# Performance work log

Measured on AMD Instinct MI355X. Metric: run time of the kernel, lower is better.

Reference implementation:

```python
import jax, jax.numpy as jnp
import numpy as np


def setup_inputs() -> dict:
    key = jax.random.key(0)
    kA, kB = jax.random.split(key)
    B, H, W, C = 8, 48, 48, 256
    feature_A = jax.random.normal(kA, (B, H, W, C), dtype=jnp.float32)
    feature_B = jax.random.normal(kB, (B, H, W, C), dtype=jnp.float32)
    return {"feature_A": feature_A, "feature_B": feature_B}


def reference(feature_A, feature_B):
    # corr[b,i,j,k,l] = mean_c A[b,i,j,c] * B[b,k,l,c]
    # Expressed as a batched GEMM over the channel dim instead of the
    # naive [B,H,W,H,W,C] broadcast intermediate.
    C = feature_A.shape[-1]
    corr = jnp.einsum('bijc,bklc->bijkl', feature_A, feature_B) / C
    # L2 norm over source positions (i,j) per target position (k,l)
    penalty = jnp.sqrt(jnp.sum(corr * corr, axis=(1, 2), keepdims=True))  # [B,1,1,H,W]
    return corr / penalty
```

## Files before the change

### kernel.cpp

```cpp
#include <hip/hip_runtime.h>
#include <hip/hip_bf16.h>


#define HW2 2304
#define CH  256
#define NB  8
#define NELEM (NB * HW2 * CH)

typedef __attribute__((ext_vector_type(8))) short bf16x8;
typedef __attribute__((ext_vector_type(4))) float f32x4;

static __device__ inline unsigned short f2bf(float f) {
    union { float f; unsigned u; } x; x.f = f;
    unsigned r = x.u + 0x7FFFu + ((x.u >> 16) & 1u);
    return (unsigned short)(r >> 16);
}

static __device__ inline void async_copy16(const void* g, void* l) {
    __builtin_amdgcn_global_load_lds(
        (const __attribute__((address_space(1))) unsigned int*)g,
        (__attribute__((address_space(3))) unsigned int*)l, 16, 0, 0);
}

__global__ __launch_bounds__(256) void convert_bf16(const float* __restrict__ A,
                                                    const float* __restrict__ B,
                                                    unsigned short* __restrict__ Abf,
                                                    unsigned short* __restrict__ Bbf) {
    const int n4 = NELEM / 4;
    for (int i = blockIdx.x * blockDim.x + threadIdx.x; i < 2 * n4;
         i += gridDim.x * blockDim.x) {
        const bool isA = i < n4;
        const int j = isA ? i : i - n4;
        float4 v = (isA ? (const float4*)A : (const float4*)B)[j];
        ushort4 p;
        p.x = f2bf(v.x); p.y = f2bf(v.y); p.z = f2bf(v.z); p.w = f2bf(v.w);
        *(ushort4*)((isA ? Abf : Bbf) + (size_t)j * 4) = p;
    }
}

template <bool WRITE_OUT>
__global__ __launch_bounds__(256) void corr_pass(const unsigned short* __restrict__ Abf,
                                                 const unsigned short* __restrict__ Bbf,
                                                 float* __restrict__ colSqG,
                                                 float* __restrict__ out) {
    __shared__ unsigned short As[2 * 128 * 32];
    __shared__ unsigned short Bs[2 * 128 * 32];
    __shared__ float colSq[128];

    const int tid = threadIdx.x;

    const int lin = blockIdx.x + 18 * (blockIdx.y + 18 * blockIdx.z);
    const int b  = lin & 7;
    const int r_ = lin >> 3;
    const int bx = r_ % 18;
    const int by = r_ / 18;

    if (!WRITE_OUT && tid < 128) colSq[tid] = 0.0f;

    const unsigned short* Ab = Abf + ((size_t)b * HW2 + (size_t)by * 128) * CH;
    const unsigned short* Bb = Bbf + ((size_t)b * HW2 + (size_t)bx * 128) * CH;

    const int srow  = tid >> 2;
    const int skcol = (tid & 3) * 8;

    const int wave = tid >> 6;
    const int lane = tid & 63;
    const int wm   = (wave >> 1) * 64;
    const int wn   = (wave & 1) * 64;
    const int lr   = lane & 15;
    const int quad = lane >> 4;
    const int k8   = quad * 8;

    f32x4 acc[4][4];
#pragma unroll
    for (int i = 0; i < 4; i++)
#pragma unroll
        for (int j = 0; j < 4; j++) acc[i][j] = (f32x4){0.f, 0.f, 0.f, 0.f};

    for (int kt = 0; kt < CH; kt += 64) {
#pragma unroll
        for (int c = 0; c < 2; c++) {
            const int kof = kt + c * 32;
#pragma unroll
            for (int i = 0; i < 2; i++) {
                async_copy16(Ab + (size_t)(srow + i * 64) * CH + kof + skcol,
                             &As[c * 4096 + tid * 8 + i * 2048]);
                async_copy16(Bb + (size_t)(srow + i * 64) * CH + kof + skcol,
                             &Bs[c * 4096 + tid * 8 + i * 2048]);
            }
        }
        __syncthreads();

#pragma unroll
        for (int c = 0; c < 2; c++) {
            bf16x8 af[4], bfr[4];
#pragma unroll
            for (int mt = 0; mt < 4; mt++)
                af[mt] = *(const bf16x8*)&As[c * 4096 + (wm + mt * 16 + lr) * 32 + k8];
#pragma unroll
            for (int nt = 0; nt < 4; nt++)
                bfr[nt] = *(const bf16x8*)&Bs[c * 4096 + (wn + nt * 16 + lr) * 32 + k8];
#pragma unroll
            for (int mt = 0; mt < 4; mt++)
#pragma unroll
                for (int nt = 0; nt < 4; nt++)
                    acc[mt][nt] = __builtin_amdgcn_mfma_f32_16x16x32_bf16(
                        af[mt], bfr[nt], acc[mt][nt], 0, 0, 0);
        }
        __syncthreads();
    }

    const int colBase = bx * 128 + wn;
    if (!WRITE_OUT) {
#pragma unroll
        for (int nt = 0; nt < 4; nt++) {
            float s = 0.f;
#pragma unroll
            for (int mt = 0; mt < 4; mt++) {
                f32x4 v = acc[mt][nt];
#pragma unroll
                for (int r = 0; r < 4; r++) s += v[r] * v[r];
            }
            s += __shfl_xor(s, 16);
            s += __shfl_xor(s, 32);
            if (quad == 0) atomicAdd(&colSq[wn + nt * 16 + lr], s);
        }
        __syncthreads();
        if (tid < 128)
            atomicAdd(&colSqG[(size_t)b * HW2 + bx * 128 + tid], colSq[tid]);
    } else {
        const size_t outBase = (size_t)b * HW2 * HW2;
#pragma unroll
        for (int nt = 0; nt < 4; nt++) {
            const int col = colBase + nt * 16 + lr;
            const float rinv = rsqrtf(colSqG[(size_t)b * HW2 + col]);
#pragma unroll
            for (int mt = 0; mt < 4; mt++) {
                const int row0 = by * 128 + wm + mt * 16 + quad * 4;
                f32x4 v = acc[mt][nt];
#pragma unroll
                for (int r = 0; r < 4; r++)
                    out[outBase + (size_t)(row0 + r) * HW2 + col] = v[r] * rinv;
            }
        }
    }
}

extern "C" void kernel_launch(void* const* d_in, const int* in_sizes, int n_in,
                              void* d_out, int out_size, void* d_ws, size_t ws_size,
                              hipStream_t stream) {
    const float* A = (const float*)d_in[0];
    const float* B = (const float*)d_in[1];
    float* out = (float*)d_out;

    unsigned short* Abf = (unsigned short*)d_ws;
    unsigned short* Bbf = Abf + NELEM;
    float* colSqG = (float*)(Bbf + NELEM);

    hipMemsetAsync(colSqG, 0, (size_t)NB * HW2 * sizeof(float), stream);
    convert_bf16<<<2048, 256, 0, stream>>>(A, B, Abf, Bbf);

    dim3 grid(HW2 / 128, HW2 / 128, NB);
    corr_pass<false><<<grid, 256, 0, stream>>>(Abf, Bbf, colSqG, out);
    corr_pass<true><<<grid, 256, 0, stream>>>(Abf, Bbf, colSqG, out);
}
```

Measured before the change: 237.5 us.

## Compute column norms via Gram matrix A^T A instead of full correlation pass

Replaces the first full HW×HW correlation GEMM used for column sum of squares with an algebraic identity: ||A b_k||^2 = b_k^T (A^T A) b_k. The convert kernel now also writes a transposed bf16 copy of A, a split-K kernel builds the 256×256 Gram matrix per batch with atomics, and a small GEMM of B against the Gram matrix gives the column norms. This removes roughly half of the MFMA work, at the cost of extra kernels, a transposed copy, and rounding the Gram matrix to bf16, which may reduce the accuracy of the norms.

After: 254.5 us. 7.2% more time.

```diff
diff --git a/kernel.cpp b/kernel.cpp
--- a/kernel.cpp
+++ b/kernel.cpp
@@ -1,11 +1,11 @@
 #include <hip/hip_runtime.h>
-#include <hip/hip_bf16.h>
 
 
 #define HW2 2304
 #define CH  256
 #define NB  8
 #define NELEM (NB * HW2 * CH)
+#define KS  6
 
 typedef __attribute__((ext_vector_type(8))) short bf16x8;
 typedef __attribute__((ext_vector_type(4))) float f32x4;
@@ -16,6 +16,11 @@
     return (unsigned short)(r >> 16);
 }
 
+static __device__ inline float bf2f(unsigned short u) {
+    union { unsigned u; float f; } x; x.u = ((unsigned)u) << 16;
+    return x.f;
+}
+
 static __device__ inline void async_copy16(const void* g, void* l) {
     __builtin_amdgcn_global_load_lds(
         (const __attribute__((address_space(1))) unsigned int*)g,
@@ -25,28 +30,203 @@
 __global__ __launch_bounds__(256) void convert_bf16(const float* __restrict__ A,
                                                     const float* __restrict__ B,
                                                     unsigned short* __restrict__ Abf,
-                                                    unsigned short* __restrict__ Bbf) {
-    const int n4 = NELEM / 4;
-    for (int i = blockIdx.x * blockDim.x + threadIdx.x; i < 2 * n4;
-         i += gridDim.x * blockDim.x) {
-        const bool isA = i < n4;
-        const int j = isA ? i : i - n4;
-        float4 v = (isA ? (const float4*)A : (const float4*)B)[j];
-        ushort4 p;
-        p.x = f2bf(v.x); p.y = f2bf(v.y); p.z = f2bf(v.z); p.w = f2bf(v.w);
-        *(ushort4*)((isA ? Abf : Bbf) + (size_t)j * 4) = p;
-    }
-}
-
-template <bool WRITE_OUT>
-__global__ __launch_bounds__(256) void corr_pass(const unsigned short* __restrict__ Abf,
-                                                 const unsigned short* __restrict__ Bbf,
-                                                 float* __restrict__ colSqG,
-                                                 float* __restrict__ out) {
+                                                    unsigned short* __restrict__ Bbf,
+                                                    unsigned short* __restrict__ Atbf) {
+    __shared__ unsigned short t[64][65];
+    const int blk = blockIdx.x;
+    const bool isA = blk < 1152;
+    const int tb = isA ? blk : blk - 1152;
+    const int b  = tb / 144;
+    const int tt = tb % 144;
+    const int ijt = tt >> 2, ct = tt & 3;
+    const size_t base = ((size_t)b * HW2 + (size_t)ijt * 64) * CH + ct * 64;
+    const float* src = (isA ? A : B) + base;
+    unsigned short* dst = (isA ? Abf : Bbf) + base;
+    const int tid = threadIdx.x;
+    const int lr = tid & 15, rq = tid >> 4;
+#pragma unroll
+    for (int p = 0; p < 4; p++) {
+        const int row = rq + p * 16;
+        float4 v = *(const float4*)(src + (size_t)row * CH + lr * 4);
+        ushort4 u;
+        u.x = f2bf(v.x); u.y = f2bf(v.y); u.z = f2bf(v.z); u.w = f2bf(v.w);
+        *(ushort4*)(dst + (size_t)row * CH + lr * 4) = u;
+        if (isA) {
+            t[row][lr * 4 + 0] = u.x; t[row][lr * 4 + 1] = u.y;
+            t[row][lr * 4 + 2] = u.z; t[row][lr * 4 + 3] = u.w;
+        }
+    }
+    if (isA) {
+        __syncthreads();
+#pragma unroll
+        for (int p = 0; p < 4; p++) {
+            const int c = rq + p * 16;
+            ushort4 u;
+            u.x = t[lr * 4 + 0][c]; u.y = t[lr * 4 + 1][c];
+            u.z = t[lr * 4 + 2][c]; u.w = t[lr * 4 + 3][c];
+            *(ushort4*)(Atbf + ((size_t)b * CH + (size_t)(ct * 64 + c)) * HW2
+                        + (size_t)ijt * 64 + lr * 4) = u;
+        }
+    }
+}
+
+__global__ __launch_bounds__(256) void gram_partial(const unsigned short* __restrict__ Atbf,
+                                                    float* __restrict__ Gf) {
     __shared__ unsigned short As[2 * 128 * 32];
     __shared__ unsigned short Bs[2 * 128 * 32];
-    __shared__ float colSq[128];
-
+    const int tid = threadIdx.x;
+    const int bx = blockIdx.x, by = blockIdx.y;
+    const int b  = blockIdx.z / KS, ks = blockIdx.z % KS;
+    const int kt0 = ks * (HW2 / KS);
+
+    const unsigned short* Ar = Atbf + ((size_t)b * CH + by * 128) * HW2;
+    const unsigned short* Br = Atbf + ((size_t)b * CH + bx * 128) * HW2;
+
+    const int srow = tid >> 2, skcol = (tid & 3) * 8;
+    const int wave = tid >> 6, lane = tid & 63;
+    const int wm = (wave >> 1) * 64, wn = (wave & 1) * 64;
+    const int lr = lane & 15, quad = lane >> 4, k8 = quad * 8;
+
+    f32x4 acc[4][4];
+#pragma unroll
+    for (int i = 0; i < 4; i++)
+#pragma unroll
+        for (int j = 0; j < 4; j++) acc[i][j] = (f32x4){0.f, 0.f, 0.f, 0.f};
+
+    for (int kt = kt0; kt < kt0 + HW2 / KS; kt += 64) {
+#pragma unroll
+        for (int c = 0; c < 2; c++) {
+            const int kof = kt + c * 32;
+#pragma unroll
+            for (int i = 0; i < 2; i++) {
+                async_copy16(Ar + (size_t)(srow + i * 64) * HW2 + kof + skcol,
+                             &As[c * 4096 + tid * 8 + i * 2048]);
+                async_copy16(Br + (size_t)(srow + i * 64) * HW2 + kof + skcol,
+                             &Bs[c * 4096 + tid * 8 + i * 2048]);
+            }
+        }
+        __syncthreads();
+#pragma unroll
+        for (int c = 0; c < 2; c++) {
+            bf16x8 af[4], bfr[4];
+#pragma unroll
+            for (int mt = 0; mt < 4; mt++)
+                af[mt] = *(const bf16x8*)&As[c * 4096 + (wm + mt * 16 + lr) * 32 + k8];
+#pragma unroll
+            for (int nt = 0; nt < 4; nt++)
+                bfr[nt] = *(const bf16x8*)&Bs[c * 4096 + (wn + nt * 16 + lr) * 32 + k8];
+#pragma unroll
+            for (int mt = 0; mt < 4; mt++)
+#pragma unroll
+                for (int nt = 0; nt < 4; nt++)
+                    acc[mt][nt] = __builtin_amdgcn_mfma_f32_16x16x32_bf16(
+                        af[mt], bfr[nt], acc[mt][nt], 0, 0, 0);
+        }
+        __syncthreads();
+    }
+#pragma unroll
+    for (int mt = 0; mt < 4; mt++)
+#pragma unroll
+        for (int nt = 0; nt < 4; nt++) {
+            f32x4 v = acc[mt][nt];
+            const int row = by * 128 + wm + mt * 16 + quad * 4;
+            const int col = bx * 128 + wn + nt * 16 + lr;
+#pragma unroll
+            for (int r = 0; r < 4; r++)
+                atomicAdd(&Gf[((size_t)b * CH + row + r) * CH + col], v[r]);
+        }
+}
+
+__global__ __launch_bounds__(256) void g_to_bf(const float* __restrict__ Gf,
+                                               unsigned short* __restrict__ Gbf) {
+    const int i = blockIdx.x * 256 + threadIdx.x;
+    float4 v = ((const float4*)Gf)[i];
+    ushort4 u;
+    u.x = f2bf(v.x); u.y = f2bf(v.y); u.z = f2bf(v.z); u.w = f2bf(v.w);
+    ((ushort4*)Gbf)[i] = u;
+}
+
+__global__ __launch_bounds__(256) void colsq_pass(const unsigned short* __restrict__ Bbf,
+                                                  const unsigned short* __restrict__ Gbf,
+                                                  float* __restrict__ colSqG) {
+    __shared__ unsigned short As[2 * 128 * 32];
+    __shared__ unsigned short Bs[2 * 128 * 32];
+    const int tid = threadIdx.x;
+    const int bx = blockIdx.x;
+    const int by = blockIdx.y;
+    const int b  = blockIdx.z;
+
+    const unsigned short* Ab = Bbf + ((size_t)b * HW2 + by * 128) * CH;
+    const unsigned short* Gb = Gbf + ((size_t)b * CH + bx * 128) * CH;
+
+    const int srow = tid >> 2, skcol = (tid & 3) * 8;
+    const int wave = tid >> 6, lane = tid & 63;
+    const int wm = (wave >> 1) * 64, wn = (wave & 1) * 64;
+    const int lr = lane & 15, quad = lane >> 4, k8 = quad * 8;
+
+    f32x4 acc[4][4];
+#pragma unroll
+    for (int i = 0; i < 4; i++)
+#pragma unroll
+        for (int j = 0; j < 4; j++) acc[i][j] = (f32x4){0.f, 0.f, 0.f, 0.f};
+
+    for (int kt = 0; kt < CH; kt += 64) {
+#pragma unroll
+        for (int c = 0; c < 2; c++) {
+            const int kof = kt + c * 32;
+#pragma unroll
+            for (int i = 0; i < 2; i++) {
+                async_copy16(Ab + (size_t)(srow + i * 64) * CH + kof + skcol,
+                             &As[c * 4096 + tid * 8 + i * 2048]);
+                async_copy16(Gb + (size_t)(srow + i * 64) * CH + kof + skcol,
+                             &Bs[c * 4096 + tid * 8 + i * 2048]);
+            }
+        }
+        __syncthreads();
+#pragma unroll
+        for (int c = 0; c < 2; c++) {
+            bf16x8 af[4], bfr[4];
+#pragma unroll
+            for (int mt = 0; mt < 4; mt++)
+                af[mt] = *(const bf16x8*)&As[c * 4096 + (wm + mt * 16 + lr) * 32 + k8];
+#pragma unroll
+            for (int nt = 0; nt < 4; nt++)
+                bfr[nt] = *(const bf16x8*)&Bs[c * 4096 + (wn + nt * 16 + lr) * 32 + k8];
+#pragma unroll
+            for (int mt = 0; mt < 4; mt++)
+#pragma unroll
+                for (int nt = 0; nt < 4; nt++)
+                    acc[mt][nt] = __builtin_amdgcn_mfma_f32_16x16x32_bf16(
+                        af[mt], bfr[nt], acc[mt][nt], 0, 0, 0);
+        }
+        __syncthreads();
+    }
+
+    const unsigned short* Brow = Ab + bx * 128;
+#pragma unroll
+    for (int mt = 0; mt < 4; mt++)
+#pragma unroll
+        for (int r = 0; r < 4; r++) {
+            const int row = wm + mt * 16 + quad * 4 + r;
+            float s = 0.f;
+#pragma unroll
+            for (int nt = 0; nt < 4; nt++) {
+                const int col = wn + nt * 16 + lr;
+                s += acc[mt][nt][r] * bf2f(Brow[(size_t)row * CH + col]);
+            }
+            s += __shfl_xor(s, 1); s += __shfl_xor(s, 2);
+            s += __shfl_xor(s, 4); s += __shfl_xor(s, 8);
+            if (lr == 0)
+                atomicAdd(&colSqG[(size_t)b * HW2 + by * 128 + row], s);
+        }
+}
+
+__global__ __launch_bounds__(256) void corr_out(const unsigned short* __restrict__ Abf,
+                                                const unsigned short* __restrict__ Bbf,
+                                                const float* __restrict__ colSqG,
+                                                float* __restrict__ out) {
+    __shared__ unsigned short As[2 * 128 * 32];
+    __shared__ unsigned short Bs[2 * 128 * 32];
     const int tid = threadIdx.x;
 
     const int lin = blockIdx.x + 18 * (blockIdx.y + 18 * blockIdx.z);
@@ -55,21 +235,13 @@
     const int bx = r_ % 18;
     const int by = r_ / 18;
 
-    if (!WRITE_OUT && tid < 128) colSq[tid] = 0.0f;
-
     const unsigned short* Ab = Abf + ((size_t)b * HW2 + (size_t)by * 128) * CH;
     const unsigned short* Bb = Bbf + ((size_t)b * HW2 + (size_t)bx * 128) * CH;
 
-    const int srow  = tid >> 2;
-    const int skcol = (tid & 3) * 8;
-
-    const int wave = tid >> 6;
-    const int lane = tid & 63;
-    const int wm   = (wave >> 1) * 64;
-    const int wn   = (wave & 1) * 64;
-    const int lr   = lane & 15;
-    const int quad = lane >> 4;
-    const int k8   = quad * 8;
+    const int srow = tid >> 2, skcol = (tid & 3) * 8;
+    const int wave = tid >> 6, lane = tid & 63;
+    const int wm = (wave >> 1) * 64, wn = (wave & 1) * 64;
+    const int lr = lane & 15, quad = lane >> 4, k8 = quad * 8;
 
     f32x4 acc[4][4];
 #pragma unroll
@@ -90,7 +262,6 @@
             }
         }
         __syncthreads();
-
 #pragma unroll
         for (int c = 0; c < 2; c++) {
             bf16x8 af[4], bfr[4];
@@ -111,37 +282,18 @@
     }
 
     const int colBase = bx * 128 + wn;
-    if (!WRITE_OUT) {
-#pragma unroll
-        for (int nt = 0; nt < 4; nt++) {
-            float s = 0.f;
-#pragma unroll
-            for (int mt = 0; mt < 4; mt++) {
-                f32x4 v = acc[mt][nt];
-#pragma unroll
-                for (int r = 0; r < 4; r++) s += v[r] * v[r];
-            }
-            s += __shfl_xor(s, 16);
-            s += __shfl_xor(s, 32);
-            if (quad == 0) atomicAdd(&colSq[wn + nt * 16 + lr], s);
-        }
-        __syncthreads();
-        if (tid < 128)
-            atomicAdd(&colSqG[(size_t)b * HW2 + bx * 128 + tid], colSq[tid]);
-    } else {
-        const size_t outBase = (size_t)b * HW2 * HW2;
-#pragma unroll
-        for (int nt = 0; nt < 4; nt++) {
-            const int col = colBase + nt * 16 + lr;
-            const float rinv = rsqrtf(colSqG[(size_t)b * HW2 + col]);
-#pragma unroll
-            for (int mt = 0; mt < 4; mt++) {
-                const int row0 = by * 128 + wm + mt * 16 + quad * 4;
-                f32x4 v = acc[mt][nt];
-#pragma unroll
-                for (int r = 0; r < 4; r++)
-                    out[outBase + (size_t)(row0 + r) * HW2 + col] = v[r] * rinv;
-            }
+    const size_t outBase = (size_t)b * HW2 * HW2;
+#pragma unroll
+    for (int nt = 0; nt < 4; nt++) {
+        const int col = colBase + nt * 16 + lr;
+        const float rinv = rsqrtf(colSqG[(size_t)b * HW2 + col]);
+#pragma unroll
+        for (int mt = 0; mt < 4; mt++) {
+            const int row0 = by * 128 + wm + mt * 16 + quad * 4;
+            f32x4 v = acc[mt][nt];
+#pragma unroll
+            for (int r = 0; r < 4; r++)
+                out[outBase + (size_t)(row0 + r) * HW2 + col] = v[r] * rinv;
         }
     }
 }
@@ -153,14 +305,19 @@
     const float* B = (const float*)d_in[1];
     float* out = (float*)d_out;
 
-    unsigned short* Abf = (unsigned short*)d_ws;
-    unsigned short* Bbf = Abf + NELEM;
-    float* colSqG = (float*)(Bbf + NELEM);
-
+    unsigned short* Abf  = (unsigned short*)d_ws;
+    unsigned short* Bbf  = Abf + NELEM;
+    unsigned short* Atbf = Bbf + NELEM;
+    unsigned short* Gbf  = Atbf + NELEM;
+    float* Gf     = (float*)(Gbf + (size_t)NB * CH * CH);
+    float* colSqG = Gf + (size_t)NB * CH * CH;
+
+    hipMemsetAsync(Gf, 0, (size_t)NB * CH * CH * sizeof(float), stream);
     hipMemsetAsync(colSqG, 0, (size_t)NB * HW2 * sizeof(float), stream);
-    convert_bf16<<<2048, 256, 0, stream>>>(A, B, Abf, Bbf);
-
-    dim3 grid(HW2 / 128, HW2 / 128, NB);
-    corr_pass<false><<<grid, 256, 0, stream>>>(Abf, Bbf, colSqG, out);
-    corr_pass<true><<<grid, 256, 0, stream>>>(Abf, Bbf, colSqG, out);
-}
+
+    convert_bf16<<<2304, 256, 0, stream>>>(A, B, Abf, Bbf, Atbf);
+    gram_partial<<<dim3(2, 2, NB * KS), 256, 0, stream>>>(Atbf, Gf);
+    g_to_bf<<<512, 256, 0, stream>>>(Gf, Gbf);
+    colsq_pass<<<dim3(2, 18, NB), 256, 0, stream>>>(Bbf, Gbf, colSqG);
+    corr_out<<<dim3(18, 18, NB), 256, 0, stream>>>(Abf, Bbf, colSqG, out);
+}
```

## Fuse norm and output passes into persistent kernel with per-group grid barrier

Applied to the files above, without the earlier changes.

Replaces the two GEMM passes (one computing column squared norms, one recomputing the GEMM to write normalized output) with a single persistent kernel of 512 blocks. Each block computes a tile, contributes its column sums of squares, waits on a per-(batch, column-block) counter until all 18 row tiles are done, then scales its accumulators in registers and writes out. This removes the second GEMM recomputation and the memset by zeroing buffers in the convert kernel. It risks spin-wait stalls and deadlock if not all blocks of a group are co-resident; an occupancy check falls back to the old path.

After: 236.8 us. Within noise of the previous version (-0.3%).

```diff
diff --git a/kernel.cpp b/kernel.cpp
--- a/kernel.cpp
+++ b/kernel.cpp
@@ -1,11 +1,13 @@
 #include <hip/hip_runtime.h>
-#include <hip/hip_bf16.h>
 
 
 #define HW2 2304
 #define CH  256
 #define NB  8
 #define NELEM (NB * HW2 * CH)
+#define NTILE 2592
+#define NGRP  144
+#define PBLK  512
 
 typedef __attribute__((ext_vector_type(8))) short bf16x8;
 typedef __attribute__((ext_vector_type(4))) float f32x4;
@@ -25,16 +27,140 @@
 __global__ __launch_bounds__(256) void convert_bf16(const float* __restrict__ A,
                                                     const float* __restrict__ B,
                                                     unsigned short* __restrict__ Abf,
-                                                    unsigned short* __restrict__ Bbf) {
+                                                    unsigned short* __restrict__ Bbf,
+                                                    float* __restrict__ colSqG,
+                                                    int* __restrict__ cnt) {
+    const int gidx = blockIdx.x * blockDim.x + threadIdx.x;
+    if (gidx < NB * HW2) colSqG[gidx] = 0.0f;
+    if (gidx < NGRP) cnt[gidx] = 0;
     const int n4 = NELEM / 4;
-    for (int i = blockIdx.x * blockDim.x + threadIdx.x; i < 2 * n4;
-         i += gridDim.x * blockDim.x) {
+    for (int i = gidx; i < 2 * n4; i += gridDim.x * blockDim.x) {
         const bool isA = i < n4;
         const int j = isA ? i : i - n4;
         float4 v = (isA ? (const float4*)A : (const float4*)B)[j];
         ushort4 p;
         p.x = f2bf(v.x); p.y = f2bf(v.y); p.z = f2bf(v.z); p.w = f2bf(v.w);
         *(ushort4*)((isA ? Abf : Bbf) + (size_t)j * 4) = p;
+    }
+}
+
+__global__ __launch_bounds__(256, 2) void corr_fused(const unsigned short* __restrict__ Abf,
+                                                     const unsigned short* __restrict__ Bbf,
+                                                     float* __restrict__ colSqG,
+                                                     int* __restrict__ cnt,
+                                                     float* __restrict__ out) {
+    __shared__ unsigned short As[2 * 128 * 32];
+    __shared__ unsigned short Bs[2 * 128 * 32];
+    __shared__ float colSq[128];
+
+    const int tid = threadIdx.x;
+    const int srow  = tid >> 2;
+    const int skcol = (tid & 3) * 8;
+    const int wave = tid >> 6, lane = tid & 63;
+    const int wm = (wave >> 1) * 64, wn = (wave & 1) * 64;
+    const int lr = lane & 15, quad = lane >> 4, k8 = quad * 8;
+
+    const int i = blockIdx.x;
+    const int T = (i & 7) * 64 + (i >> 3);
+
+    for (int t = T; t < NTILE; t += PBLK) {
+        const int g  = t / 18;
+        const int by = t % 18;
+        const int b  = g / 18;
+        const int bx = g % 18;
+
+        const unsigned short* Ab = Abf + ((size_t)b * HW2 + (size_t)by * 128) * CH;
+        const unsigned short* Bb = Bbf + ((size_t)b * HW2 + (size_t)bx * 128) * CH;
+
+        if (tid < 128) colSq[tid] = 0.0f;
+
+        f32x4 acc[4][4];
+#pragma unroll
+        for (int mi = 0; mi < 4; mi++)
+#pragma unroll
+            for (int nj = 0; nj < 4; nj++) acc[mi][nj] = (f32x4){0.f, 0.f, 0.f, 0.f};
+
+        for (int kt = 0; kt < CH; kt += 64) {
+#pragma unroll
+            for (int c = 0; c < 2; c++) {
+                const int kof = kt + c * 32;
+#pragma unroll
+                for (int ii = 0; ii < 2; ii++) {
+                    async_copy16(Ab + (size_t)(srow + ii * 64) * CH + kof + skcol,
+                                 &As[c * 4096 + tid * 8 + ii * 2048]);
+                    async_copy16(Bb + (size_t)(srow + ii * 64) * CH + kof + skcol,
+                                 &Bs[c * 4096 + tid * 8 + ii * 2048]);
+                }
+            }
+            __syncthreads();
+#pragma unroll
+            for (int c = 0; c < 2; c++) {
+                bf16x8 af[4], bfr[4];
+#pragma unroll
+                for (int mt = 0; mt < 4; mt++)
+                    af[mt] = *(const bf16x8*)&As[c * 4096 + (wm + mt * 16 + lr) * 32 + k8];
+#pragma unroll
+                for (int nt = 0; nt < 4; nt++)
+                    bfr[nt] = *(const bf16x8*)&Bs[c * 4096 + (wn + nt * 16 + lr) * 32 + k8];
+#pragma unroll
+                for (int mt = 0; mt < 4; mt++)
+#pragma unroll
+                    for (int nt = 0; nt < 4; nt++)
+                        acc[mt][nt] = __builtin_amdgcn_mfma_f32_16x16x32_bf16(
+                            af[mt], bfr[nt], acc[mt][nt], 0, 0, 0);
+            }
+            __syncthreads();
+        }
+
+#pragma unroll
+        for (int nt = 0; nt < 4; nt++) {
+            float s = 0.f;
+#pragma unroll
+            for (int mt = 0; mt < 4; mt++) {
+                f32x4 v = acc[mt][nt];
+#pragma unroll
+                for (int r = 0; r < 4; r++) s += v[r] * v[r];
+            }
+            s += __shfl_xor(s, 16);
+            s += __shfl_xor(s, 32);
+            if (quad == 0) atomicAdd(&colSq[wn + nt * 16 + lr], s);
+        }
+        __syncthreads();
+        if (tid < 128)
+            atomicAdd(&colSqG[(size_t)b * HW2 + bx * 128 + tid], colSq[tid]);
+        __syncthreads();
+
+        if (tid == 0) {
+            __hip_atomic_fetch_add(&cnt[g], 1, __ATOMIC_ACQ_REL,
+                                   __HIP_MEMORY_SCOPE_AGENT);
+            while (__hip_atomic_load(&cnt[g], __ATOMIC_ACQUIRE,
+                                     __HIP_MEMORY_SCOPE_AGENT) < 18)
+                __builtin_amdgcn_s_sleep(8);
+        }
+        __syncthreads();
+
+        if (tid < 128)
+            colSq[tid] = __hip_atomic_fetch_add(
+                &colSqG[(size_t)b * HW2 + bx * 128 + tid], 0.0f,
+                __ATOMIC_RELAXED, __HIP_MEMORY_SCOPE_AGENT);
+        __syncthreads();
+
+        const size_t outBase = (size_t)b * HW2 * HW2;
+#pragma unroll
+        for (int nt = 0; nt < 4; nt++) {
+            const int colL = wn + nt * 16 + lr;
+            const int col  = bx * 128 + colL;
+            const float rinv = rsqrtf(colSq[colL]);
+#pragma unroll
+            for (int mt = 0; mt < 4; mt++) {
+                const int row0 = by * 128 + wm + mt * 16 + quad * 4;
+                f32x4 v = acc[mt][nt];
+#pragma unroll
+                for (int r = 0; r < 4; r++)
+                    out[outBase + (size_t)(row0 + r) * HW2 + col] = v[r] * rinv;
+            }
+        }
+        __syncthreads();
     }
 }
 
@@ -48,7 +174,6 @@
     __shared__ float colSq[128];
 
     const int tid = threadIdx.x;
-
     const int lin = blockIdx.x + 18 * (blockIdx.y + 18 * blockIdx.z);
     const int b  = lin & 7;
     const int r_ = lin >> 3;
@@ -62,14 +187,9 @@
 
     const int srow  = tid >> 2;
     const int skcol = (tid & 3) * 8;
-
-    const int wave = tid >> 6;
-    const int lane = tid & 63;
-    const int wm   = (wave >> 1) * 64;
-    const int wn   = (wave & 1) * 64;
-    const int lr   = lane & 15;
-    const int quad = lane >> 4;
-    const int k8   = quad * 8;
+    const int wave = tid >> 6, lane = tid & 63;
+    const int wm = (wave >> 1) * 64, wn = (wave & 1) * 64;
+    const int lr = lane & 15, quad = lane >> 4, k8 = quad * 8;
 
     f32x4 acc[4][4];
 #pragma unroll
@@ -90,7 +210,6 @@
             }
         }
         __syncthreads();
-
 #pragma unroll
         for (int c = 0; c < 2; c++) {
             bf16x8 af[4], bfr[4];
@@ -156,11 +275,23 @@
     unsigned short* Abf = (unsigned short*)d_ws;
     unsigned short* Bbf = Abf + NELEM;
     float* colSqG = (float*)(Bbf + NELEM);
-
-    hipMemsetAsync(colSqG, 0, (size_t)NB * HW2 * sizeof(float), stream);
-    convert_bf16<<<2048, 256, 0, stream>>>(A, B, Abf, Bbf);
-
-    dim3 grid(HW2 / 128, HW2 / 128, NB);
-    corr_pass<false><<<grid, 256, 0, stream>>>(Abf, Bbf, colSqG, out);
-    corr_pass<true><<<grid, 256, 0, stream>>>(Abf, Bbf, colSqG, out);
-}
+    int* cnt = (int*)(colSqG + (size_t)NB * HW2);
+
+    static int occ = -1;
+    if (occ < 0) {
+        int n = 0;
+        hipError_t e = hipOccupancyMaxActiveBlocksPerMultiprocessor(
+            &n, (const void*)corr_fused, 256, 0);
+        occ = (e == hipSuccess) ? n : 2;
+    }
+
+    convert_bf16<<<2048, 256, 0, stream>>>(A, B, Abf, Bbf, colSqG, cnt);
+
+    if (occ >= 2) {
+        corr_fused<<<PBLK, 256, 0, stream>>>(Abf, Bbf, colSqG, cnt, out);
+    } else {
+        dim3 grid(HW2 / 128, HW2 / 128, NB);
+        corr_pass<false><<<grid, 256, 0, stream>>>(Abf, Bbf, colSqG, out);
+        corr_pass<true><<<grid, 256, 0, stream>>>(Abf, Bbf, colSqG, out);
+    }
+}
```

## Compute correlation GEMM once, then normalize the output in a separate pass

Applied to the files above, without the earlier changes.

Replaces the two-pass scheme (one GEMM pass for column norms, a second GEMM pass to write normalized output) with a single GEMM pass. That pass writes raw correlations and accumulates the column sums of squares. A new elementwise kernel then rescales the output in place by the inverse column norms. The memset is folded into the conversion kernel. This removes the duplicated matrix multiply, but adds an extra full read and write of the large output buffer.

New measurement: 259.1 us. 9.1% more time.

```diff
diff --git a/kernel.cpp b/kernel.cpp
--- a/kernel.cpp
+++ b/kernel.cpp
@@ -1,5 +1,4 @@
 #include <hip/hip_runtime.h>
-#include <hip/hip_bf16.h>
 
 
 #define HW2 2304
@@ -25,10 +24,12 @@
 __global__ __launch_bounds__(256) void convert_bf16(const float* __restrict__ A,
                                                     const float* __restrict__ B,
                                                     unsigned short* __restrict__ Abf,
-                                                    unsigned short* __restrict__ Bbf) {
+                                                    unsigned short* __restrict__ Bbf,
+                                                    float* __restrict__ colSqG) {
+    const int gidx = blockIdx.x * blockDim.x + threadIdx.x;
+    if (gidx < NB * HW2) colSqG[gidx] = 0.0f;
     const int n4 = NELEM / 4;
-    for (int i = blockIdx.x * blockDim.x + threadIdx.x; i < 2 * n4;
-         i += gridDim.x * blockDim.x) {
+    for (int i = gidx; i < 2 * n4; i += gridDim.x * blockDim.x) {
         const bool isA = i < n4;
         const int j = isA ? i : i - n4;
         float4 v = (isA ? (const float4*)A : (const float4*)B)[j];
@@ -38,11 +39,10 @@
     }
 }
 
-template <bool WRITE_OUT>
-__global__ __launch_bounds__(256) void corr_pass(const unsigned short* __restrict__ Abf,
-                                                 const unsigned short* __restrict__ Bbf,
-                                                 float* __restrict__ colSqG,
-                                                 float* __restrict__ out) {
+__global__ __launch_bounds__(256) void corr_raw(const unsigned short* __restrict__ Abf,
+                                                const unsigned short* __restrict__ Bbf,
+                                                float* __restrict__ colSqG,
+                                                float* __restrict__ out) {
     __shared__ unsigned short As[2 * 128 * 32];
     __shared__ unsigned short Bs[2 * 128 * 32];
     __shared__ float colSq[128];
@@ -55,21 +55,16 @@
     const int bx = r_ % 18;
     const int by = r_ / 18;
 
-    if (!WRITE_OUT && tid < 128) colSq[tid] = 0.0f;
+    if (tid < 128) colSq[tid] = 0.0f;
 
     const unsigned short* Ab = Abf + ((size_t)b * HW2 + (size_t)by * 128) * CH;
     const unsigned short* Bb = Bbf + ((size_t)b * HW2 + (size_t)bx * 128) * CH;
 
     const int srow  = tid >> 2;
     const int skcol = (tid & 3) * 8;
-
-    const int wave = tid >> 6;
-    const int lane = tid & 63;
-    const int wm   = (wave >> 1) * 64;
-    const int wn   = (wave & 1) * 64;
-    const int lr   = lane & 15;
-    const int quad = lane >> 4;
-    const int k8   = quad * 8;
+    const int wave = tid >> 6, lane = tid & 63;
+    const int wm = (wave >> 1) * 64, wn = (wave & 1) * 64;
+    const int lr = lane & 15, quad = lane >> 4, k8 = quad * 8;
 
     f32x4 acc[4][4];
 #pragma unroll
@@ -90,7 +85,6 @@
             }
         }
         __syncthreads();
-
 #pragma unroll
         for (int c = 0; c < 2; c++) {
             bf16x8 af[4], bfr[4];
@@ -110,39 +104,53 @@
         __syncthreads();
     }
 
-    const int colBase = bx * 128 + wn;
-    if (!WRITE_OUT) {
+    const size_t outBase = (size_t)b * HW2 * HW2;
 #pragma unroll
-        for (int nt = 0; nt < 4; nt++) {
-            float s = 0.f;
+    for (int nt = 0; nt < 4; nt++) {
+        const int col = bx * 128 + wn + nt * 16 + lr;
 #pragma unroll
-            for (int mt = 0; mt < 4; mt++) {
-                f32x4 v = acc[mt][nt];
+        for (int mt = 0; mt < 4; mt++) {
+            const int row0 = by * 128 + wm + mt * 16 + quad * 4;
+            f32x4 v = acc[mt][nt];
 #pragma unroll
-                for (int r = 0; r < 4; r++) s += v[r] * v[r];
-            }
-            s += __shfl_xor(s, 16);
-            s += __shfl_xor(s, 32);
-            if (quad == 0) atomicAdd(&colSq[wn + nt * 16 + lr], s);
+            for (int r = 0; r < 4; r++)
+                out[outBase + (size_t)(row0 + r) * HW2 + col] = v[r];
         }
-        __syncthreads();
-        if (tid < 128)
-            atomicAdd(&colSqG[(size_t)b * HW2 + bx * 128 + tid], colSq[tid]);
-    } else {
-        const size_t outBase = (size_t)b * HW2 * HW2;
+    }
+
 #pragma unroll
-        for (int nt = 0; nt < 4; nt++) {
-            const int col = colBase + nt * 16 + lr;
-            const float rinv = rsqrtf(colSqG[(size_t)b * HW2 + col]);
+    for (int nt = 0; nt < 4; nt++) {
+        float s = 0.f;
 #pragma unroll
-            for (int mt = 0; mt < 4; mt++) {
-                const int row0 = by * 128 + wm + mt * 16 + quad * 4;
-                f32x4 v = acc[mt][nt];
+        for (int mt = 0; mt < 4; mt++) {
+            f32x4 v = acc[mt][nt];
 #pragma unroll
-                for (int r = 0; r < 4; r++)
-                    out[outBase + (size_t)(row0 + r) * HW2 + col] = v[r] * rinv;
-            }
+            for (int r = 0; r < 4; r++) s += v[r] * v[r];
         }
+        s += __shfl_xor(s, 16);
+        s += __shfl_xor(s, 32);
+        if (quad == 0) atomicAdd(&colSq[wn + nt * 16 + lr], s);
+    }
+    __syncthreads();
+    if (tid < 128)
+        atomicAdd(&colSqG[(size_t)b * HW2 + bx * 128 + tid], colSq[tid]);
+}
+
+__global__ __launch_bounds__(256) void normalize(float* __restrict__ out,
+                                                 const float* __restrict__ colSqG) {
+    const int total = NB * HW2 * (HW2 / 4);
+    for (int i = blockIdx.x * blockDim.x + threadIdx.x; i < total;
+         i += gridDim.x * blockDim.x) {
+        float4 v = ((const float4*)out)[i];
+        const int e   = i * 4;
+        const int col = e % HW2;
+        const int b   = i / (HW2 * (HW2 / 4));
+        float4 c = *(const float4*)(colSqG + b * HW2 + col);
+        v.x *= rsqrtf(c.x);
+        v.y *= rsqrtf(c.y);
+        v.z *= rsqrtf(c.z);
+        v.w *= rsqrtf(c.w);
+        ((float4*)out)[i] = v;
     }
 }
 
@@ -157,10 +165,10 @@
     unsigned short* Bbf = Abf + NELEM;
     float* colSqG = (float*)(Bbf + NELEM);
 
-    hipMemsetAsync(colSqG, 0, (size_t)NB * HW2 * sizeof(float), stream);
-    convert_bf16<<<2048, 256, 0, stream>>>(A, B, Abf, Bbf);
+    convert_bf16<<<2048, 256, 0, stream>>>(A, B, Abf, Bbf, colSqG);
 
     dim3 grid(HW2 / 128, HW2 / 128, NB);
-    corr_pass<false><<<grid, 256, 0, stream>>>(Abf, Bbf, colSqG, out);
-    corr_pass<true><<<grid, 256, 0, stream>>>(Abf, Bbf, colSqG, out);
+    corr_raw<<<grid, 256, 0, stream>>>(Abf, Bbf, colSqG, out);
+
+    normalize<<<2048, 256, 0, stream>>>(out, colSqG);
 }
```
